# Performance work log

Measured on AMD Instinct MI355X. Metric: run time of the kernel, lower is better.

Reference implementation:

```python
import jax, jax.numpy as jnp
import numpy as np

# Default bone connections from BoneLengthLoss.__init__
BONES = np.array([(1, 2), (1, 3), (1, 4), (2, 5), (3, 6), (11, 12), (11, 13), (12, 14),
                  (13, 14), (14, 15), (15, 16), (16, 17), (12, 18), (18, 20), (20, 22),
                  (13, 19), (19, 21), (21, 23), (16, 24), (16, 25), (24, 26), (25, 26),
                  (24, 27), (27, 29), (29, 31), (25, 28), (28, 30), (30, 32), (17, 33),
                  (33, 34), (34, 35), (35, 36)], dtype=np.int32)
J1 = jnp.asarray(BONES[:, 0])
J2 = jnp.asarray(BONES[:, 1])

BATCH = 524288
NUM_KPTS = 37


def setup_inputs() -> dict:
    key = jax.random.key(0)
    k1, k2, k3 = jax.random.split(key, 3)
    pose_3d_pred = jax.random.normal(k1, (BATCH, NUM_KPTS, 3), dtype=jnp.float32)
    pose_3d_ref = jax.random.normal(k2, (BATCH, NUM_KPTS, 3), dtype=jnp.float32)
    valid_mask = jax.random.randint(k3, (BATCH, NUM_KPTS), 0, 2).astype(jnp.bool_)
    return {"pose_3d_pred": pose_3d_pred, "pose_3d_ref": pose_3d_ref,
            "valid_mask": valid_mask}


def reference(pose_3d_pred, pose_3d_ref, valid_mask):
    # Gather both endpoints of every bone: (B, n_bones, 3)
    pred_vec = pose_3d_pred[:, J2, :] - pose_3d_pred[:, J1, :]
    ref_vec = pose_3d_ref[:, J2, :] - pose_3d_ref[:, J1, :]
    pred_len = jnp.linalg.norm(pred_vec, axis=-1)  # (B, n_bones)
    ref_len = jnp.linalg.norm(ref_vec, axis=-1)    # (B, n_bones)
    # Bone is valid iff both endpoints are valid
    bone_valid = (valid_mask[:, J1] & valid_mask[:, J2]).astype(pred_len.dtype)
    # MSE over all valid (batch, bone) entries == mean over concatenated valid lengths
    sq_err = (pred_len - ref_len) ** 2
    num = jnp.sum(sq_err * bone_valid)
    den = jnp.sum(bone_valid)
    return num / den
```

## Files before the change

### kernel.cpp

```cpp
#include <hip/hip_runtime.h>


#define NBONES  32
#define NKPT    37
#define ROWF    (NKPT * 3)
#define NB      32
#define BLOCK   256
#define TILE_F  (NB * ROWF)
#define TILE_V4 (TILE_F / 4)
#define TILE_M  (NB * NKPT)
#define TILE_MW (TILE_M / 4)

__constant__ unsigned char c_j1[NBONES] = {1,1,1,2,3,11,11,12,13,14,15,16,12,18,20,13,19,21,16,16,24,25,24,27,29,25,28,30,17,33,34,35};
__constant__ unsigned char c_j2[NBONES] = {2,3,4,5,6,12,13,14,14,15,16,17,18,20,22,19,21,23,24,25,26,26,27,29,31,28,30,32,33,34,35,36};

__global__ void detect_mask_layout(const unsigned int* __restrict__ mw, int nwords,
                                   unsigned int* __restrict__ ws) {
    unsigned int local = 0;
    for (int i = blockIdx.x * blockDim.x + threadIdx.x; i < nwords;
         i += gridDim.x * blockDim.x)
        local |= mw[i] & 0xFFFFFF00u;
    if (__any(local != 0) && (threadIdx.x & 63) == 0)
        atomicOr(&ws[2], 1u);
}

__global__ __launch_bounds__(BLOCK, 4)
void bone_main(const float* __restrict__ pred, const float* __restrict__ ref,
               const void* __restrict__ mask, int B, unsigned int* __restrict__ ws) {
    __shared__ float4 s_pred[TILE_V4];
    __shared__ float4 s_ref[TILE_V4];
    __shared__ unsigned int s_mask_w[TILE_MW];
    __shared__ float s_rednum[BLOCK / 64];
    __shared__ unsigned int s_redden[BLOCK / 64];

    const int tid  = threadIdx.x;
    const int lrow = tid >> 3;
    const int grp  = tid & 7;

    const bool mask_bytes = (ws[2] != 0);

    int j1v[4], j2v[4];
#pragma unroll
    for (int k = 0; k < 4; ++k) {
        j1v[k] = (int)c_j1[grp * 4 + k] * 3;
        j2v[k] = (int)c_j2[grp * 4 + k] * 3;
    }
    int m1v[4], m2v[4];
#pragma unroll
    for (int k = 0; k < 4; ++k) {
        m1v[k] = (int)c_j1[grp * 4 + k];
        m2v[k] = (int)c_j2[grp * 4 + k];
    }

    const float4* __restrict__ pred4 = (const float4*)pred;
    const float4* __restrict__ ref4  = (const float4*)ref;
    const unsigned int* __restrict__ mw = (const unsigned int*)mask;
    const int* __restrict__ mi = (const int*)mask;

    float num = 0.0f;
    unsigned int den = 0u;

    const int ntiles = B / NB;
    for (int tile = blockIdx.x; tile < ntiles; tile += gridDim.x) {
        const int base4 = tile * TILE_V4;
#pragma unroll
        for (int it = 0; it < (TILE_V4 + BLOCK - 1) / BLOCK; ++it) {
            int i = tid + it * BLOCK;
            if (i < TILE_V4) {
                s_pred[i] = pred4[base4 + i];
                s_ref[i]  = ref4[base4 + i];
            }
        }
        if (mask_bytes) {
            const int mb = tile * TILE_MW;
            for (int i = tid; i < TILE_MW; i += BLOCK)
                s_mask_w[i] = mw[mb + i];
        } else {
            const int mb = tile * TILE_M;
            unsigned char* sb = (unsigned char*)s_mask_w;
            for (int i = tid; i < TILE_M; i += BLOCK)
                sb[i] = (unsigned char)mi[mb + i];
        }
        __syncthreads();

        const float* sp = (const float*)s_pred + lrow * ROWF;
        const float* sr = (const float*)s_ref  + lrow * ROWF;
        const unsigned char* sm = (const unsigned char*)s_mask_w + lrow * NKPT;
#pragma unroll
        for (int k = 0; k < 4; ++k) {
            const int a = j1v[k], b = j2v[k];
            float dx = sp[b] - sp[a], dy = sp[b + 1] - sp[a + 1], dz = sp[b + 2] - sp[a + 2];
            float pl = sqrtf(dx * dx + dy * dy + dz * dz);
            float ex = sr[b] - sr[a], ey = sr[b + 1] - sr[a + 1], ez = sr[b + 2] - sr[a + 2];
            float rl = sqrtf(ex * ex + ey * ey + ez * ez);
            unsigned int v = (unsigned int)(sm[m1v[k]] & sm[m2v[k]]);
            float d = pl - rl;
            num += v ? d * d : 0.0f;
            den += v;
        }
        __syncthreads();
    }

#pragma unroll
    for (int off = 32; off > 0; off >>= 1) {
        num += __shfl_down(num, off, 64);
        den += __shfl_down(den, off, 64);
    }
    const int wave = tid >> 6, lane = tid & 63;
    if (lane == 0) { s_rednum[wave] = num; s_redden[wave] = den; }
    __syncthreads();
    if (tid == 0) {
        float n = 0.0f;
        unsigned int d = 0u;
#pragma unroll
        for (int w = 0; w < BLOCK / 64; ++w) { n += s_rednum[w]; d += s_redden[w]; }
        atomicAdd((float*)&ws[0], n);
        atomicAdd(&ws[1], d);
    }
}

__global__ void finalize(const unsigned int* __restrict__ ws, float* __restrict__ out) {
    out[0] = ((const float*)ws)[0] / (float)ws[1];
}

extern "C" void kernel_launch(void* const* d_in, const int* in_sizes, int n_in,
                              void* d_out, int out_size, void* d_ws, size_t ws_size,
                              hipStream_t stream) {
    const float* pred = (const float*)d_in[0];
    const float* ref  = (const float*)d_in[1];
    const void*  mask = d_in[2];
    const int n_mask  = in_sizes[2];
    const int B       = n_mask / NKPT;
    unsigned int* ws  = (unsigned int*)d_ws;

    hipMemsetAsync(d_ws, 0, 16, stream);
    detect_mask_layout<<<256, BLOCK, 0, stream>>>(
        (const unsigned int*)mask, n_mask / 4, ws);
    bone_main<<<2048, BLOCK, 0, stream>>>(pred, ref, mask, B, ws);
    finalize<<<1, 1, 0, stream>>>(ws, (float*)d_out);
}
```

Baseline: 565.8 us.

## Use per-wave tiles without block barriers and fuse init/finalize into fewer launches

Each wave now processes its own 8-row tile. It loads the tile into registers, stores it to a private LDS region and computes on it, so the block-wide __syncthreads inside the loop are gone. The memset, the full-mask layout scan and the finalize kernel are replaced by a one-block init kernel that samples only the first 1024 mask words, plus a last-block-done atomic that writes the result. Together these remove launch overhead and barrier stalls. The sampled layout detection could misclassify masks whose nonzero high bytes only appear later in the array.

```diff
diff --git a/kernel.cpp b/kernel.cpp
--- a/kernel.cpp
+++ b/kernel.cpp
@@ -1,55 +1,52 @@
 #include <hip/hip_runtime.h>
 
 
-#define NBONES  32
-#define NKPT    37
-#define ROWF    (NKPT * 3)
-#define NB      32
-#define BLOCK   256
-#define TILE_F  (NB * ROWF)
-#define TILE_V4 (TILE_F / 4)
-#define TILE_M  (NB * NKPT)
-#define TILE_MW (TILE_M / 4)
+#define NBONES 32
+#define NKPT   37
+#define ROWF   111
+#define RPW    8
+#define WT_F4  222
+#define WT_MW  74
+#define WT_MI  296
+#define BLOCK  256
+#define WPB    4
+#define GRID   2048
 
 __constant__ unsigned char c_j1[NBONES] = {1,1,1,2,3,11,11,12,13,14,15,16,12,18,20,13,19,21,16,16,24,25,24,27,29,25,28,30,17,33,34,35};
 __constant__ unsigned char c_j2[NBONES] = {2,3,4,5,6,12,13,14,14,15,16,17,18,20,22,19,21,23,24,25,26,26,27,29,31,28,30,32,33,34,35,36};
 
-__global__ void detect_mask_layout(const unsigned int* __restrict__ mw, int nwords,
-                                   unsigned int* __restrict__ ws) {
+__global__ void init_detect(const unsigned int* __restrict__ mw,
+                            unsigned int* __restrict__ ws) {
+    const int tid = threadIdx.x;
+    if (tid < 4) ws[tid] = 0u;
+    __syncthreads();
     unsigned int local = 0;
-    for (int i = blockIdx.x * blockDim.x + threadIdx.x; i < nwords;
-         i += gridDim.x * blockDim.x)
-        local |= mw[i] & 0xFFFFFF00u;
-    if (__any(local != 0) && (threadIdx.x & 63) == 0)
-        atomicOr(&ws[2], 1u);
+    for (int i = tid; i < 1024; i += BLOCK) local |= mw[i] & 0xFFFFFF00u;
+    if (__any(local != 0) && (tid & 63) == 0) atomicOr(&ws[2], 1u);
 }
 
 __global__ __launch_bounds__(BLOCK, 4)
 void bone_main(const float* __restrict__ pred, const float* __restrict__ ref,
-               const void* __restrict__ mask, int B, unsigned int* __restrict__ ws) {
-    __shared__ float4 s_pred[TILE_V4];
-    __shared__ float4 s_ref[TILE_V4];
-    __shared__ unsigned int s_mask_w[TILE_MW];
-    __shared__ float s_rednum[BLOCK / 64];
-    __shared__ unsigned int s_redden[BLOCK / 64];
+               const void* __restrict__ mask, int B,
+               unsigned int* __restrict__ ws, float* __restrict__ out) {
+    __shared__ __align__(16) float s_pose[WPB][2][RPW * ROWF];
+    __shared__ __align__(4) unsigned char s_mask[WPB][WT_MI + 8];
+    __shared__ float s_rn[WPB];
+    __shared__ unsigned int s_rd[WPB];
 
     const int tid  = threadIdx.x;
-    const int lrow = tid >> 3;
-    const int grp  = tid & 7;
+    const int wave = tid >> 6;
+    const int lane = tid & 63;
+    const int row  = lane >> 3;
+    const int grp  = lane & 7;
 
     const bool mask_bytes = (ws[2] != 0);
 
     int j1v[4], j2v[4];
 #pragma unroll
     for (int k = 0; k < 4; ++k) {
-        j1v[k] = (int)c_j1[grp * 4 + k] * 3;
-        j2v[k] = (int)c_j2[grp * 4 + k] * 3;
-    }
-    int m1v[4], m2v[4];
-#pragma unroll
-    for (int k = 0; k < 4; ++k) {
-        m1v[k] = (int)c_j1[grp * 4 + k];
-        m2v[k] = (int)c_j2[grp * 4 + k];
+        j1v[k] = (int)c_j1[grp * 4 + k];
+        j2v[k] = (int)c_j2[grp * 4 + k];
     }
 
     const float4* __restrict__ pred4 = (const float4*)pred;
@@ -57,48 +54,73 @@
     const unsigned int* __restrict__ mw = (const unsigned int*)mask;
     const int* __restrict__ mi = (const int*)mask;
 
+    float*  sp_w = &s_pose[wave][0][0];
+    float*  sr_w = &s_pose[wave][1][0];
+    float4* sp4  = (float4*)sp_w;
+    float4* sr4  = (float4*)sr_w;
+    unsigned char* sm_w = &s_mask[wave][0];
+
     float num = 0.0f;
     unsigned int den = 0u;
 
-    const int ntiles = B / NB;
-    for (int tile = blockIdx.x; tile < ntiles; tile += gridDim.x) {
-        const int base4 = tile * TILE_V4;
+    const int nwt    = B / RPW;
+    const int gwave  = blockIdx.x * WPB + wave;
+    const int nwaves = GRID * WPB;
+
+    int idx[4];
 #pragma unroll
-        for (int it = 0; it < (TILE_V4 + BLOCK - 1) / BLOCK; ++it) {
-            int i = tid + it * BLOCK;
-            if (i < TILE_V4) {
-                s_pred[i] = pred4[base4 + i];
-                s_ref[i]  = ref4[base4 + i];
+    for (int j = 0; j < 4; ++j) idx[j] = min(lane + 64 * j, WT_F4 - 1);
+
+    for (int wt = gwave; wt < nwt; wt += nwaves) {
+        const float4* pb = pred4 + (size_t)wt * WT_F4;
+        const float4* rb = ref4  + (size_t)wt * WT_F4;
+
+        float4 vp[4], vr[4];
+#pragma unroll
+        for (int j = 0; j < 4; ++j) vp[j] = pb[idx[j]];
+#pragma unroll
+        for (int j = 0; j < 4; ++j) vr[j] = rb[idx[j]];
+
+        if (mask_bytes) {
+            const unsigned int* mb = mw + (size_t)wt * WT_MW;
+            unsigned int m0 = mb[lane];
+            int i1 = min(lane + 64, WT_MW - 1);
+            unsigned int m1 = mb[i1];
+            ((unsigned int*)sm_w)[lane] = m0;
+            ((unsigned int*)sm_w)[i1]   = m1;
+        } else {
+            const int* mb = mi + (size_t)wt * WT_MI;
+#pragma unroll
+            for (int j = 0; j < 5; ++j) {
+                int i = min(lane + 64 * j, WT_MI - 1);
+                sm_w[i] = (unsigned char)mb[i];
             }
         }
-        if (mask_bytes) {
-            const int mb = tile * TILE_MW;
-            for (int i = tid; i < TILE_MW; i += BLOCK)
-                s_mask_w[i] = mw[mb + i];
-        } else {
-            const int mb = tile * TILE_M;
-            unsigned char* sb = (unsigned char*)s_mask_w;
-            for (int i = tid; i < TILE_M; i += BLOCK)
-                sb[i] = (unsigned char)mi[mb + i];
-        }
-        __syncthreads();
 
-        const float* sp = (const float*)s_pred + lrow * ROWF;
-        const float* sr = (const float*)s_ref  + lrow * ROWF;
-        const unsigned char* sm = (const unsigned char*)s_mask_w + lrow * NKPT;
+#pragma unroll
+        for (int j = 0; j < 4; ++j) sp4[idx[j]] = vp[j];
+#pragma unroll
+        for (int j = 0; j < 4; ++j) sr4[idx[j]] = vr[j];
+
+        const float* sp = sp_w + row * ROWF;
+        const float* sr = sr_w + row * ROWF;
+        const unsigned char* sm = sm_w + row * NKPT;
 #pragma unroll
         for (int k = 0; k < 4; ++k) {
-            const int a = j1v[k], b = j2v[k];
-            float dx = sp[b] - sp[a], dy = sp[b + 1] - sp[a + 1], dz = sp[b + 2] - sp[a + 2];
+            const int a3 = j1v[k] * 3, b3 = j2v[k] * 3;
+            float dx = sp[b3] - sp[a3];
+            float dy = sp[b3 + 1] - sp[a3 + 1];
+            float dz = sp[b3 + 2] - sp[a3 + 2];
             float pl = sqrtf(dx * dx + dy * dy + dz * dz);
-            float ex = sr[b] - sr[a], ey = sr[b + 1] - sr[a + 1], ez = sr[b + 2] - sr[a + 2];
+            float ex = sr[b3] - sr[a3];
+            float ey = sr[b3 + 1] - sr[a3 + 1];
+            float ez = sr[b3 + 2] - sr[a3 + 2];
             float rl = sqrtf(ex * ex + ey * ey + ez * ez);
-            unsigned int v = (unsigned int)(sm[m1v[k]] & sm[m2v[k]]);
+            unsigned int v = (unsigned int)(sm[j1v[k]] & sm[j2v[k]]);
             float d = pl - rl;
             num += v ? d * d : 0.0f;
             den += v;
         }
-        __syncthreads();
     }
 
 #pragma unroll
@@ -106,21 +128,21 @@
         num += __shfl_down(num, off, 64);
         den += __shfl_down(den, off, 64);
     }
-    const int wave = tid >> 6, lane = tid & 63;
-    if (lane == 0) { s_rednum[wave] = num; s_redden[wave] = den; }
+    if (lane == 0) { s_rn[wave] = num; s_rd[wave] = den; }
     __syncthreads();
     if (tid == 0) {
-        float n = 0.0f;
-        unsigned int d = 0u;
-#pragma unroll
-        for (int w = 0; w < BLOCK / 64; ++w) { n += s_rednum[w]; d += s_redden[w]; }
+        float n = s_rn[0] + s_rn[1] + s_rn[2] + s_rn[3];
+        unsigned int d = s_rd[0] + s_rd[1] + s_rd[2] + s_rd[3];
         atomicAdd((float*)&ws[0], n);
         atomicAdd(&ws[1], d);
+        __threadfence();
+        unsigned int prev = atomicAdd(&ws[3], 1u);
+        if (prev == (unsigned int)(gridDim.x - 1)) {
+            float fn = atomicAdd((float*)&ws[0], 0.0f);
+            unsigned int fd = atomicAdd(&ws[1], 0u);
+            out[0] = fn / (float)fd;
+        }
     }
-}
-
-__global__ void finalize(const unsigned int* __restrict__ ws, float* __restrict__ out) {
-    out[0] = ((const float*)ws)[0] / (float)ws[1];
 }
 
 extern "C" void kernel_launch(void* const* d_in, const int* in_sizes, int n_in,
@@ -133,9 +155,6 @@
     const int B       = n_mask / NKPT;
     unsigned int* ws  = (unsigned int*)d_ws;
 
-    hipMemsetAsync(d_ws, 0, 16, stream);
-    detect_mask_layout<<<256, BLOCK, 0, stream>>>(
-        (const unsigned int*)mask, n_mask / 4, ws);
-    bone_main<<<2048, BLOCK, 0, stream>>>(pred, ref, mask, B, ws);
-    finalize<<<1, 1, 0, stream>>>(ws, (float*)d_out);
+    init_detect<<<1, BLOCK, 0, stream>>>((const unsigned int*)mask, ws);
+    bone_main<<<GRID, BLOCK, 0, stream>>>(pred, ref, mask, B, ws, (float*)d_out);
 }
```

After: 582.8 us. 1.03x slower.
